# Optimization experiments

Hardware: AMD Instinct MI355X
Metric: run time of the kernel (lower is better)

Reference implementation:

```python
import jax, jax.numpy as jnp
from jax import lax
import numpy as np

B, T = 32, 64
E = 64        # embed_dim
U = 32        # num_measurements
D0, D1 = 300, 100
S = 9         # speaker_num
CELL = 64     # output_cell_dim
C = 6         # n_classes
EPS = 1e-12


def setup_inputs() -> dict:
    key = jax.random.key(0)
    ks = jax.random.split(key, 16)
    sc = 1.0 / np.sqrt(E)
    n = lambda i, shape, s=1.0: (jax.random.normal(ks[i], shape, jnp.float32) * s)
    return {
        "x0": n(0, (B, T, D0)),
        "x1": n(1, (B, T, D1)),
        "smask": jax.random.uniform(ks[2], (B, T, S), jnp.float32),
        "umask": jnp.ones((B, T), jnp.float32),
        "W_ih0": n(3, (4 * E, D0), sc), "W_hh0": n(4, (4 * E, E), sc),
        "b_ih0": n(5, (4 * E,), sc), "b_hh0": n(6, (4 * E,), sc),
        "W_ih1": n(7, (4 * E, D1), sc), "W_hh1": n(8, (4 * E, E), sc),
        "b_ih1": n(9, (4 * E,), sc), "b_hh1": n(10, (4 * E,), sc),
        "phase_table": jax.random.uniform(ks[11], (S, E), jnp.float32, -np.pi, np.pi),
        "meas_kernel": jax.random.uniform(ks[12], (U, E, 2), jnp.float32),
        "W1": n(13, (CELL, 2 * U), 0.1), "b1": jnp.zeros((CELL,), jnp.float32),
        "W2": n(14, (C, CELL), 0.1), "b2": jnp.zeros((C,), jnp.float32),
    }


def _lstm_tanh(x, um, Wih, Whh, bih, bhh):
    # torch.nn.LSTMCell (gate order i,f,g,o) + extra tanh applied to h each step;
    # the tanh-ed h is carried as the recurrent state (dropout = identity in eval).
    b, t, _ = x.shape
    e = Whh.shape[1]

    def step(carry, inp):
        h, c = carry
        xt, ut = inp
        g = (xt * ut[:, None]) @ Wih.T + bih + h @ Whh.T + bhh
        i, f, gg, o = jnp.split(g, 4, axis=-1)
        c = jax.nn.sigmoid(f) * c + jax.nn.sigmoid(i) * jnp.tanh(gg)
        h = jnp.tanh(jax.nn.sigmoid(o) * jnp.tanh(c))
        return (h, c), h

    h0 = jnp.zeros((b, e), x.dtype)
    _, hs = lax.scan(step, (h0, h0), (jnp.swapaxes(x, 0, 1), um.T))
    return jnp.swapaxes(hs, 0, 1)  # (B,T,E)


def _measure(amp, phase, kernel):
    # pure state v = cos(phase)*amp + i sin(phase)*amp; rho = |v><v|
    r = jnp.cos(phase) * amp
    im = jnp.sin(phase) * amp
    rho_r = jnp.einsum('bti,btj->btij', r, r) + jnp.einsum('bti,btj->btij', im, im)
    rho_i = jnp.einsum('bti,btj->btij', im, r) - jnp.einsum('bti,btj->btij', r, im)
    u = kernel.shape[0]
    norm = jnp.clip(jnp.linalg.norm(kernel.reshape(u, -1), axis=-1), EPS)
    kn = kernel / norm[:, None, None]
    kr, ki = kn[..., 0], kn[..., 1]
    Pr = jnp.einsum('ui,uj->uij', kr, kr) + jnp.einsum('ui,uj->uij', ki, ki)
    Pi = jnp.einsum('ui,uj->uij', ki, kr) - jnp.einsum('ui,uj->uij', kr, ki)
    return jnp.einsum('btij,uij->btu', rho_r, Pr) - jnp.einsum('btij,uij->btu', rho_i, Pi)


def reference(x0, x1, smask, umask, W_ih0, W_hh0, b_ih0, b_hh0,
              W_ih1, W_hh1, b_ih1, b_hh1, phase_table, meas_kernel,
              W1, b1, W2, b2):
    h0 = _lstm_tanh(x0, umask, W_ih0, W_hh0, b_ih0, b_hh0)
    h1 = _lstm_tanh(x1, umask, W_ih1, W_hh1, b_ih1, b_hh1)
    norm = lambda h: h / jnp.clip(jnp.linalg.norm(h, axis=-1, keepdims=True), EPS)
    phase = phase_table[jnp.argmax(smask, axis=-1)]  # (B,T,E); table shared by both modalities
    m = jnp.concatenate([_measure(norm(h0), phase, meas_kernel),
                         _measure(norm(h1), phase, meas_kernel)], axis=-1)
    hid = jax.nn.relu(m @ W1.T + b1)
    pred = jnp.tanh(hid @ W2.T + b2)
    return jax.nn.log_softmax(pred, axis=2)
```

## Files before the change

### kernel.cpp

```cpp
#include <hip/hip_runtime.h>

typedef unsigned short ushort_t;
typedef unsigned int uint_t;

__device__ __forceinline__ float bf2f(ushort_t v) {
  union { uint_t u; float f; } x; x.u = ((uint_t)v) << 16; return x.f;
}
__device__ __forceinline__ float lo16(uint_t u) {
  union { uint_t u; float f; } x; x.u = u << 16; return x.f;
}
__device__ __forceinline__ float hi16(uint_t u) {
  union { uint_t u; float f; } x; x.u = u & 0xffff0000u; return x.f;
}
__device__ __forceinline__ ushort_t f2bf(float f) {
  union { float f; uint_t u; } x; x.f = f;
  uint_t u = x.u;
  uint_t r = (u + 0x7fffu + ((u >> 16) & 1u)) >> 16;
  return (ushort_t)r;
}
__device__ __forceinline__ bool is_bf16(const void* um) {
  return *(const uint_t*)um == 0x3F803F80u;
}
__device__ __forceinline__ float ld_dual(const void* p, int i, bool isb) {
  return isb ? bf2f(((const ushort_t*)p)[i]) : ((const float*)p)[i];
}
__device__ __forceinline__ float fsig(float x) { return 1.f / (1.f + __expf(-x)); }
__device__ __forceinline__ float ftanh(float x) { return 2.f / (1.f + __expf(-2.f * x)) - 1.f; }

template <int D, bool ISB>
__device__ __forceinline__ void proj_body(
    const void* __restrict__ x, const void* __restrict__ um,
    const void* __restrict__ Wih, const void* __restrict__ bih,
    const void* __restrict__ bhh, float* __restrict__ xw, float* xs)
{
  const int tid = threadIdx.x;
  const int r0 = blockIdx.x * 8;
  for (int i = tid; i < 8 * D; i += 256) {
    const int r = i / D;
    xs[i] = ld_dual(x, r0 * D + i, ISB) * ld_dual(um, r0 + r, ISB);
  }
  __syncthreads();
  float acc[8];
#pragma unroll
  for (int r = 0; r < 8; ++r) acc[r] = 0.f;
#pragma unroll 5
  for (int k = 0; k < D; k += 4) {
    float w0, w1, w2, w3;
    if (ISB) {
      const ushort_t* wr = (const ushort_t*)Wih + tid * D;
      const uint2 wu = *(const uint2*)(wr + k);
      w0 = lo16(wu.x); w1 = hi16(wu.x); w2 = lo16(wu.y); w3 = hi16(wu.y);
    } else {
      const float* wr = (const float*)Wih + tid * D;
      const float4 wv = *(const float4*)(wr + k);
      w0 = wv.x; w1 = wv.y; w2 = wv.z; w3 = wv.w;
    }
#pragma unroll
    for (int r = 0; r < 8; ++r) {
      const float4 xv = *(const float4*)(xs + r * D + k);
      acc[r] = fmaf(xv.x, w0, acc[r]);
      acc[r] = fmaf(xv.y, w1, acc[r]);
      acc[r] = fmaf(xv.z, w2, acc[r]);
      acc[r] = fmaf(xv.w, w3, acc[r]);
    }
  }
  const float bias = ld_dual(bih, tid, ISB) + ld_dual(bhh, tid, ISB);
  const int pos = ((tid & 63) << 2) | (tid >> 6);
#pragma unroll
  for (int r = 0; r < 8; ++r)
    xw[(r0 + r) * 256 + pos] = acc[r] + bias;
}

__global__ __launch_bounds__(256) void proj_both(
    const void* __restrict__ x0, const void* __restrict__ x1,
    const void* __restrict__ um,
    const void* __restrict__ Wih0, const void* __restrict__ bih0,
    const void* __restrict__ bhh0,
    const void* __restrict__ Wih1, const void* __restrict__ bih1,
    const void* __restrict__ bhh1,
    float* __restrict__ xw0, float* __restrict__ xw1)
{
  __shared__ __align__(16) float xs[8 * 300];
  const bool isb = is_bf16(um);
  if (blockIdx.y == 0) {
    if (isb) proj_body<300, true>(x0, um, Wih0, bih0, bhh0, xw0, xs);
    else     proj_body<300, false>(x0, um, Wih0, bih0, bhh0, xw0, xs);
  } else {
    if (isb) proj_body<100, true>(x1, um, Wih1, bih1, bhh1, xw1, xs);
    else     proj_body<100, false>(x1, um, Wih1, bih1, bhh1, xw1, xs);
  }
}

__global__ __launch_bounds__(256) void lstm_k(
    const float* __restrict__ xw0, const float* __restrict__ xw1,
    const void* __restrict__ Whh0, const void* __restrict__ Whh1,
    const void* __restrict__ um,
    float* __restrict__ h0r, float* __restrict__ h1r)
{
  const int bid = blockIdx.x;
  const int l = bid >> 5;
  const int b = bid & 31;
  const float* xw = (l ? xw1 : xw0) + b * 64 * 256;
  const void* Whh = (l ? Whh1 : Whh0);
  float* hr = (l ? h1r : h0r) + b * 64 * 64;
  const int tid = threadIdx.x;
  const int e = tid >> 2;
  const int q = tid & 3;
  const int k0 = q << 4;
  const bool isb = is_bf16(um);

  float w[4][16];
  if (isb) {
#pragma unroll
    for (int t = 0; t < 4; ++t) {
      const ushort_t* wr = (const ushort_t*)Whh + (t * 64 + e) * 64 + k0;
#pragma unroll
      for (int j = 0; j < 16; j += 8) {
        const uint4 v = *(const uint4*)(wr + j);
        w[t][j + 0] = lo16(v.x); w[t][j + 1] = hi16(v.x);
        w[t][j + 2] = lo16(v.y); w[t][j + 3] = hi16(v.y);
        w[t][j + 4] = lo16(v.z); w[t][j + 5] = hi16(v.z);
        w[t][j + 6] = lo16(v.w); w[t][j + 7] = hi16(v.w);
      }
    }
  } else {
#pragma unroll
    for (int t = 0; t < 4; ++t) {
      const float* wr = (const float*)Whh + (t * 64 + e) * 64 + k0;
#pragma unroll
      for (int j = 0; j < 16; j += 4) {
        const float4 v = *(const float4*)(wr + j);
        w[t][j + 0] = v.x; w[t][j + 1] = v.y;
        w[t][j + 2] = v.z; w[t][j + 3] = v.w;
      }
    }
  }
  __shared__ __align__(16) float hsh[2][64];
  if (tid < 64) hsh[0][tid] = 0.f;
  __syncthreads();
  float c = 0.f;
  float gin = xw[tid];
  for (int s = 0; s < 64; ++s) {
    const float gnext = xw[((s + 1) & 63) * 256 + tid];
    const float* hp = hsh[s & 1] + k0;
    float p0 = 0.f, p1 = 0.f, p2 = 0.f, p3 = 0.f;
#pragma unroll
    for (int j = 0; j < 16; j += 4) {
      const float4 hv = *(const float4*)(hp + j);
      p0 = fmaf(w[0][j + 0], hv.x, p0); p0 = fmaf(w[0][j + 1], hv.y, p0);
      p0 = fmaf(w[0][j + 2], hv.z, p0); p0 = fmaf(w[0][j + 3], hv.w, p0);
      p1 = fmaf(w[1][j + 0], hv.x, p1); p1 = fmaf(w[1][j + 1], hv.y, p1);
      p1 = fmaf(w[1][j + 2], hv.z, p1); p1 = fmaf(w[1][j + 3], hv.w, p1);
      p2 = fmaf(w[2][j + 0], hv.x, p2); p2 = fmaf(w[2][j + 1], hv.y, p2);
      p2 = fmaf(w[2][j + 2], hv.z, p2); p2 = fmaf(w[2][j + 3], hv.w, p2);
      p3 = fmaf(w[3][j + 0], hv.x, p3); p3 = fmaf(w[3][j + 1], hv.y, p3);
      p3 = fmaf(w[3][j + 2], hv.z, p3); p3 = fmaf(w[3][j + 3], hv.w, p3);
    }
    if (q == 0) p0 += gin;
    else if (q == 1) p1 += gin;
    else if (q == 2) p2 += gin;
    else p3 += gin;
    p0 += __shfl_xor(p0, 1); p0 += __shfl_xor(p0, 2);
    p1 += __shfl_xor(p1, 1); p1 += __shfl_xor(p1, 2);
    p2 += __shfl_xor(p2, 1); p2 += __shfl_xor(p2, 2);
    p3 += __shfl_xor(p3, 1); p3 += __shfl_xor(p3, 2);
    const float yi = fsig(p0);
    const float yf = fsig(p1);
    const float yg = ftanh(p2);
    const float yo = fsig(p3);
    c = fmaf(yf, c, yi * yg);
    const float h = ftanh(yo * ftanh(c));
    if (q == 0) {
      hsh[(s + 1) & 1][e] = h;
      hr[s * 64 + e] = h;
    }
    __syncthreads();
    gin = gnext;
  }
}

__global__ __launch_bounds__(256) void head_k(
    const float* __restrict__ h0r, const float* __restrict__ h1r,
    const void* __restrict__ smask, const void* __restrict__ um,
    const void* __restrict__ ptab, const void* __restrict__ mker,
    const void* __restrict__ W1, const void* __restrict__ b1,
    const void* __restrict__ W2, const void* __restrict__ b2,
    void* __restrict__ out)
{
  __shared__ float2 knT[64][32];
  __shared__ float w1T[64][64];
  __shared__ float w2T[64][8];
  __shared__ float b1s[64];
  __shared__ float b2s[8];
  __shared__ float rim[4][4][64];
  __shared__ float msh[4][64];
  __shared__ float hidsh[4][64];
  __shared__ float psh[4][8];

  const int tid = threadIdx.x;
  const bool isb = is_bf16(um);
  {
    const int u = tid >> 3, sub = tid & 7;
    float vr[8], vi[8];
    float ssq = 0.f;
#pragma unroll
    for (int q = 0; q < 8; ++q) {
      const int e = sub * 8 + q;
      if (isb) {
        const uint_t kk = ((const uint_t*)mker)[u * 64 + e];
        vr[q] = lo16(kk); vi[q] = hi16(kk);
      } else {
        const float2 kk = ((const float2*)mker)[u * 64 + e];
        vr[q] = kk.x; vi[q] = kk.y;
      }
      ssq = fmaf(vr[q], vr[q], ssq);
      ssq = fmaf(vi[q], vi[q], ssq);
    }
    ssq += __shfl_xor(ssq, 1);
    ssq += __shfl_xor(ssq, 2);
    ssq += __shfl_xor(ssq, 4);
    const float rn = 1.f / fmaxf(sqrtf(ssq), 1e-12f);
#pragma unroll
    for (int q = 0; q < 8; ++q) {
      const int e = sub * 8 + q;
      knT[e][u] = make_float2(vr[q] * rn, vi[q] * rn);
    }
  }
  for (int i = tid; i < 4096; i += 256) {
    const int j = i >> 6, ll = i & 63;
    w1T[ll][j] = ld_dual(W1, i, isb);
  }
  if (tid < 64) b1s[tid] = ld_dual(b1, tid, isb);
  for (int i = tid; i < 384; i += 256) {
    const int cc = i >> 6, j = i & 63;
    w2T[j][cc] = ld_dual(W2, i, isb);
  }
  if (tid < 6) b2s[tid] = ld_dual(b2, tid, isb);
  __syncthreads();

  const int wv = tid >> 6, lane = tid & 63;
  const int item = blockIdx.x * 4 + wv;
  const float h0raw = h0r[item * 64 + lane];
  const float h1raw = h1r[item * 64 + lane];
  float ss0 = h0raw * h0raw, ss1 = h1raw * h1raw;
#pragma unroll
  for (int m = 1; m < 64; m <<= 1) {
    ss0 += __shfl_xor(ss0, m);
    ss1 += __shfl_xor(ss1, m);
  }
  const float h0 = h0raw / fmaxf(sqrtf(ss0), 1e-12f);
  const float h1 = h1raw / fmaxf(sqrtf(ss1), 1e-12f);

  int idx = 0;
  if (lane == 0) {
    float best = -1e30f;
#pragma unroll
    for (int si = 0; si < 9; ++si) {
      const float v = ld_dual(smask, item * 9 + si, isb);
      if (v > best) { best = v; idx = si; }
    }
  }
  idx = __shfl(idx, 0, 64);
  const float ph = ld_dual(ptab, idx * 64 + lane, isb);
  float sr, cr;
  __sincosf(ph, &sr, &cr);
  rim[wv][0][lane] = cr * h0;
  rim[wv][1][lane] = sr * h0;
  rim[wv][2][lane] = cr * h1;
  rim[wv][3][lane] = sr * h1;
  __syncthreads();
  {
    const int u = lane & 31;
    const float* ra = rim[wv][(lane >= 32) ? 2 : 0];
    const float* ia = rim[wv][(lane >= 32) ? 3 : 1];
    float ar = 0.f, ai = 0.f;
#pragma unroll 8
    for (int e = 0; e < 64; ++e) {
      const float2 k = knT[e][u];
      const float rr = ra[e], ii = ia[e];
      ar = fmaf(rr, k.x, ar);
      ar = fmaf(-ii, k.y, ar);
      ai = fmaf(rr, k.y, ai);
      ai = fmaf(ii, k.x, ai);
    }
    msh[wv][lane] = fmaf(ar, ar, ai * ai);
  }
  __syncthreads();
  {
    float acc = b1s[lane];
#pragma unroll 8
    for (int L = 0; L < 64; ++L)
      acc = fmaf(msh[wv][L], w1T[L][lane], acc);
    hidsh[wv][lane] = fmaxf(acc, 0.f);
  }
  __syncthreads();
  if (lane < 6) {
    float a2 = b2s[lane];
#pragma unroll 8
    for (int j = 0; j < 64; ++j)
      a2 = fmaf(hidsh[wv][j], w2T[j][lane], a2);
    psh[wv][lane] = ftanh(a2);
  }
  __syncthreads();
  if (lane < 6) {
    const float p = psh[wv][lane];
    float mx = psh[wv][0];
#pragma unroll
    for (int cc = 1; cc < 6; ++cc) mx = fmaxf(mx, psh[wv][cc]);
    float sum = 0.f;
#pragma unroll
    for (int cc = 0; cc < 6; ++cc) sum += __expf(psh[wv][cc] - mx);
    const float res = p - mx - __logf(sum);
    if (isb) ((ushort_t*)out)[item * 6 + lane] = f2bf(res);
    else     ((float*)out)[item * 6 + lane] = res;
  }
}

extern "C" void kernel_launch(void* const* d_in, const int* in_sizes, int n_in,
                              void* d_out, int out_size, void* d_ws, size_t ws_size,
                              hipStream_t stream)
{
  (void)in_sizes; (void)n_in; (void)out_size; (void)ws_size;
  const void* x0    = d_in[0];
  const void* x1    = d_in[1];
  const void* smask = d_in[2];
  const void* um    = d_in[3];
  const void* Wih0  = d_in[4];
  const void* Whh0  = d_in[5];
  const void* bih0  = d_in[6];
  const void* bhh0  = d_in[7];
  const void* Wih1  = d_in[8];
  const void* Whh1  = d_in[9];
  const void* bih1  = d_in[10];
  const void* bhh1  = d_in[11];
  const void* ptab  = d_in[12];
  const void* mker  = d_in[13];
  const void* W1    = d_in[14];
  const void* b1    = d_in[15];
  const void* W2    = d_in[16];
  const void* b2    = d_in[17];

  float* xw0 = (float*)d_ws;
  float* xw1 = xw0 + 2048 * 256;
  float* h0r = xw1 + 2048 * 256;
  float* h1r = h0r + 2048 * 64;

  hipLaunchKernelGGL(proj_both, dim3(256, 2), dim3(256), 0, stream,
                     x0, x1, um, Wih0, bih0, bhh0, Wih1, bih1, bhh1,
                     xw0, xw1);
  hipLaunchKernelGGL(lstm_k, dim3(64), dim3(256), 0, stream,
                     xw0, xw1, Whh0, Whh1, um, h0r, h1r);
  hipLaunchKernelGGL(head_k, dim3(512), dim3(256), 0, stream,
                     h0r, h1r, smask, um, ptab, mker, W1, b1, W2, b2,
                     d_out);
}
```

Baseline: 173.9 us.

## Stage LSTM input gates and hidden history in LDS, use DPP reductions

```diff
diff --git a/kernel.cpp b/kernel.cpp
--- a/kernel.cpp
+++ b/kernel.cpp
@@ -26,6 +26,15 @@
 }
 __device__ __forceinline__ float fsig(float x) { return 1.f / (1.f + __expf(-x)); }
 __device__ __forceinline__ float ftanh(float x) { return 2.f / (1.f + __expf(-2.f * x)) - 1.f; }
+
+__device__ __forceinline__ float dpp_add_xor1(float v) {
+  const int r = __builtin_amdgcn_update_dpp(0, __float_as_int(v), 0xB1, 0xF, 0xF, true);
+  return v + __int_as_float(r);
+}
+__device__ __forceinline__ float dpp_add_xor2(float v) {
+  const int r = __builtin_amdgcn_update_dpp(0, __float_as_int(v), 0x4E, 0xF, 0xF, true);
+  return v + __int_as_float(r);
+}
 
 template <int D, bool ISB>
 __device__ __forceinline__ void proj_body(
@@ -91,12 +100,15 @@
   }
 }
 
-__global__ __launch_bounds__(256) void lstm_k(
+__global__ __launch_bounds__(256, 1) void lstm_k(
     const float* __restrict__ xw0, const float* __restrict__ xw1,
     const void* __restrict__ Whh0, const void* __restrict__ Whh1,
     const void* __restrict__ um,
     float* __restrict__ h0r, float* __restrict__ h1r)
 {
+  __shared__ __align__(16) float xws[64 * 256];
+  __shared__ __align__(16) float hist[65 * 64];
+
   const int bid = blockIdx.x;
   const int l = bid >> 5;
   const int b = bid & 31;
@@ -109,6 +121,10 @@
   const int k0 = q << 4;
   const bool isb = is_bf16(um);
 
+  for (int i = tid; i < 4096; i += 256)
+    *(float4*)(xws + i * 4) = *(const float4*)(xw + i * 4);
+  if (tid < 64) hist[tid] = 0.f;
+
   float w[4][16];
   if (isb) {
 #pragma unroll
@@ -135,14 +151,12 @@
       }
     }
   }
-  __shared__ __align__(16) float hsh[2][64];
-  if (tid < 64) hsh[0][tid] = 0.f;
-  __syncthreads();
+  __syncthreads();
+
   float c = 0.f;
-  float gin = xw[tid];
   for (int s = 0; s < 64; ++s) {
-    const float gnext = xw[((s + 1) & 63) * 256 + tid];
-    const float* hp = hsh[s & 1] + k0;
+    const float gin = xws[s * 256 + tid];
+    const float* hp = hist + s * 64 + k0;
     float p0 = 0.f, p1 = 0.f, p2 = 0.f, p3 = 0.f;
 #pragma unroll
     for (int j = 0; j < 16; j += 4) {
@@ -160,23 +174,21 @@
     else if (q == 1) p1 += gin;
     else if (q == 2) p2 += gin;
     else p3 += gin;
-    p0 += __shfl_xor(p0, 1); p0 += __shfl_xor(p0, 2);
-    p1 += __shfl_xor(p1, 1); p1 += __shfl_xor(p1, 2);
-    p2 += __shfl_xor(p2, 1); p2 += __shfl_xor(p2, 2);
-    p3 += __shfl_xor(p3, 1); p3 += __shfl_xor(p3, 2);
+    p0 = dpp_add_xor1(p0); p0 = dpp_add_xor2(p0);
+    p1 = dpp_add_xor1(p1); p1 = dpp_add_xor2(p1);
+    p2 = dpp_add_xor1(p2); p2 = dpp_add_xor2(p2);
+    p3 = dpp_add_xor1(p3); p3 = dpp_add_xor2(p3);
     const float yi = fsig(p0);
     const float yf = fsig(p1);
     const float yg = ftanh(p2);
     const float yo = fsig(p3);
     c = fmaf(yf, c, yi * yg);
     const float h = ftanh(yo * ftanh(c));
-    if (q == 0) {
-      hsh[(s + 1) & 1][e] = h;
-      hr[s * 64 + e] = h;
-    }
+    if (q == 0) hist[(s + 1) * 64 + e] = h;
     __syncthreads();
-    gin = gnext;
-  }
+  }
+  for (int i = tid; i < 1024; i += 256)
+    *(float4*)(hr + i * 4) = *(const float4*)(hist + 64 + i * 4);
 }
 
 __global__ __launch_bounds__(256) void head_k(
@@ -204,26 +216,26 @@
     float vr[8], vi[8];
     float ssq = 0.f;
 #pragma unroll
-    for (int q = 0; q < 8; ++q) {
-      const int e = sub * 8 + q;
+    for (int qq = 0; qq < 8; ++qq) {
+      const int e = sub * 8 + qq;
       if (isb) {
         const uint_t kk = ((const uint_t*)mker)[u * 64 + e];
-        vr[q] = lo16(kk); vi[q] = hi16(kk);
+        vr[qq] = lo16(kk); vi[qq] = hi16(kk);
       } else {
         const float2 kk = ((const float2*)mker)[u * 64 + e];
-        vr[q] = kk.x; vi[q] = kk.y;
+        vr[qq] = kk.x; vi[qq] = kk.y;
       }
-      ssq = fmaf(vr[q], vr[q], ssq);
-      ssq = fmaf(vi[q], vi[q], ssq);
+      ssq = fmaf(vr[qq], vr[qq], ssq);
+      ssq = fmaf(vi[qq], vi[qq], ssq);
     }
     ssq += __shfl_xor(ssq, 1);
     ssq += __shfl_xor(ssq, 2);
     ssq += __shfl_xor(ssq, 4);
     const float rn = 1.f / fmaxf(sqrtf(ssq), 1e-12f);
 #pragma unroll
-    for (int q = 0; q < 8; ++q) {
-      const int e = sub * 8 + q;
-      knT[e][u] = make_float2(vr[q] * rn, vi[q] * rn);
+    for (int qq = 0; qq < 8; ++qq) {
+      const int e = sub * 8 + qq;
+      knT[e][u] = make_float2(vr[qq] * rn, vi[qq] * rn);
     }
   }
   for (int i = tid; i < 4096; i += 256) {
```

New measurement: 165.4 us. 1.05x faster.
